# Optimization experiments

Hardware: AMD Instinct MI355X
Metric: run time of the kernel (lower is better)

## Reference

```python
import jax, jax.numpy as jnp
import numpy as np

B, T, C, A, D, H, W = 2, 16, 64, 64, 32, 32, 32  # batch, timepoints, channels, att_features, spatial


def setup_inputs() -> dict:
    key = jax.random.key(0)
    ks = jax.random.split(key, 7)
    s = 1.0 / np.sqrt(C)
    return {
        "x": jax.random.normal(ks[0], (B, T, C, D, H, W), dtype=jnp.float32),
        "Wk": jax.random.normal(ks[1], (A, C), dtype=jnp.float32) * s,
        "bk": jax.random.normal(ks[2], (A,), dtype=jnp.float32) * s,
        "Wq": jax.random.normal(ks[3], (A, C), dtype=jnp.float32) * s,
        "bq": jax.random.normal(ks[4], (A,), dtype=jnp.float32) * s,
        "Wv": jax.random.normal(ks[5], (C, C), dtype=jnp.float32) * s,
        "bv": jax.random.normal(ks[6], (C,), dtype=jnp.float32) * s,
    }


def reference(x, Wk, bk, Wq, bq, Wv, bv):
    # kernel=1 Conv3d == pointwise channel mixing. Project and move spatial
    # dims to the front exactly like movedim((3,4,5),(1,2,3)):
    # result layout [B, D, H, W, T, out_ch].
    def proj(Wt, bt):
        return jnp.einsum('btcdhw,oc->bdhwto', x, Wt) + bt

    k = proj(Wk, bk)  # [B,D,H,W,T,A]
    q = proj(Wq, bq)  # [B,D,H,W,T,A]
    v = proj(Wv, bv)  # [B,D,H,W,T,C]

    scale = 1.0 / np.sqrt(float(Wk.shape[0]))  # sqrt(att_features)
    att = jnp.einsum('bdhwta,bdhwsa->bdhwts', k, q) * scale  # [B,D,H,W,T,T]
    # norm = partial(softmax, dim=1) on the 6-D tensor -> softmax over spatial D axis
    att_map = jax.nn.softmax(att, axis=1)

    # features = (value^T @ att_map)^T: feat[...,s,c] = sum_t v[...,t,c] * att_map[...,t,s]
    feat = jnp.einsum('bdhwtc,bdhwts->bdhwsc', v, att_map)  # [B,D,H,W,T,C]
    # movedim((1,2,3),(3,4,5)): back to [B, T, C, D, H, W]
    return jnp.transpose(feat, (0, 4, 5, 1, 2, 3))
```

## Files before the change

### kernel.cpp

```cpp
#include <hip/hip_runtime.h>

typedef short v8s __attribute__((ext_vector_type(8)));
typedef float v4f __attribute__((ext_vector_type(4)));
typedef float v2f __attribute__((ext_vector_type(2)));

#define NSP 32768
#define XSTR 2056
#define WS_ZP_B 65536ull

__device__ __forceinline__ unsigned short f2bf(float f) {
  union { float f; unsigned u; } v; v.f = f;
  unsigned r = v.u + 0x7fffu + ((v.u >> 16) & 1u);
  return (unsigned short)(r >> 16);
}
__device__ __forceinline__ unsigned pk(float a, float b) {
  return (unsigned)f2bf(a) | ((unsigned)f2bf(b) << 16);
}

union UF8 { v8s v; unsigned u[4]; uint4 q; };


__global__ __launch_bounds__(512) void prep_kernel(
    const float* __restrict__ Wk, const float* __restrict__ bk,
    const float* __restrict__ Wq, const float* __restrict__ bq,
    const float* __restrict__ Wv, unsigned* __restrict__ ws) {
  __shared__ float sWk[4096], sWq[4096], sWv[4096], sbk[64], sbq[64];
  for (int i = threadIdx.x; i < 4096; i += 512) { sWk[i] = Wk[i]; sWq[i] = Wq[i]; sWv[i] = Wv[i]; }
  if (threadIdx.x < 64) { sbk[threadIdx.x] = bk[threadIdx.x]; sbq[threadIdx.x] = bq[threadIdx.x]; }
  __syncthreads();
  for (int task = threadIdx.x; task < 18 * 64; task += 512) {
    int f = task >> 6, lane = task & 63;
    int i16 = lane & 15, g = lane >> 4;
    unsigned short e[8];
    #pragma unroll
    for (int j = 0; j < 8; ++j) {
      int k = (((j >> 2) << 4) + 4 * g + (j & 3));
      float acc = 0.f;
      if (f < 8) {
        int row = ((f >> 1) << 4) + i16;
        int cc  = ((f & 1) << 5) + k;
        for (int a = 0; a < 64; ++a) acc += sWk[a * 64 + row] * sWq[a * 64 + cc];
      } else if (f < 10) {
        int c = ((f - 8) << 5) + k;
        if (i16 == 0)      { for (int a = 0; a < 64; ++a) acc += sWk[a * 64 + c] * sbq[a]; }
        else if (i16 == 1) { for (int a = 0; a < 64; ++a) acc += sbk[a] * sWq[a * 64 + c]; }
      } else {
        int c  = (((f - 10) >> 1) << 4) + i16;
        int cp = (((f - 10) & 1) << 5) + k;
        acc = sWv[c * 64 + cp];
      }
      e[j] = f2bf(acc);
    }
    unsigned* dst = ws + (size_t)(f * 64 + lane) * 4;
    dst[0] = e[0] | ((unsigned)e[1] << 16);
    dst[1] = e[2] | ((unsigned)e[3] << 16);
    dst[2] = e[4] | ((unsigned)e[5] << 16);
    dst[3] = e[6] | ((unsigned)e[7] << 16);
  }
  if (threadIdx.x == 0) {
    float beta = 0.f;
    for (int a = 0; a < 64; ++a) beta += sbk[a] * sbq[a];
    ((float*)ws)[18 * 256] = beta;
  }
}

#define S2L 0.18033688011112042f

#define DECODE256() \
  int bid = (int)blockIdx.x; \
  int b = bid & 1, dc = (bid >> 1) & 3, h = bid >> 3; \
  const int d0 = dc << 3; \
  const size_t base0 = (size_t)b * 33554432 + h * 32;

#define DECODE512() \
  int bid = (int)blockIdx.x; \
  int b = bid & 1, dcc = (bid >> 1) & 7, h = bid >> 4; \
  const int d0 = dcc << 2; \
  const size_t base0 = (size_t)b * 33554432 + h * 32;

#define STAGE_DEFS(BUF) \
  const int w2 = tid & 15; \
  const int rp0 = tid >> 4; \
  v2f sA[16], sB[16]; \
  auto issueH = [&](int d, int half) { \
    const float* xp = x + base0 + (size_t)d * 1024; \
    _Pragma("unroll") \
    for (int i = 0; i < 8; ++i) { \
      int rp = half * 256 + (i << 5) + rp0; \
      const float* r0 = xp + (size_t)(2 * rp) * NSP + 2 * w2; \
      sA[half * 8 + i] = *(const v2f*)r0; \
      sB[half * 8 + i] = *(const v2f*)(r0 + NSP); \
    } \
  }; \
  auto writeH = [&](int half) { \
    _Pragma("unroll") \
    for (int i = 0; i < 8; ++i) { \
      int rp = half * 256 + (i << 5) + rp0; \
      int t = rp >> 5, c = (rp & 31) << 1; \
      int off = (t << 7) + (((c << 1)) ^ ((t & 7) << 4)); \
      *(unsigned*)(&BUF[(2 * w2) * XSTR + off])     = pk(sA[half * 8 + i].x, sB[half * 8 + i].x); \
      *(unsigned*)(&BUF[(2 * w2 + 1) * XSTR + off]) = pk(sA[half * 8 + i].y, sB[half * 8 + i].y); \
    } \
  };

#define LOADX_DEF(BUF) \
  auto loadX = [&](int loc, v8s fX[2]) { \
    const unsigned char* bp = &BUF[loc * XSTR + (i16 << 7)]; \
    const int sw = (i16 & 7) << 4; \
    _Pragma("unroll") \
    for (int kc = 0; kc < 2; ++kc) { \
      union { v8s v; unsigned long long dd[2]; } u; \
      int o = (kc << 6) + (g << 3); \
      u.dd[0] = *(const unsigned long long*)(bp + (o ^ sw)); \
      u.dd[1] = *(const unsigned long long*)(bp + ((o + 32) ^ sw)); \
      fX[kc] = u.v; \
    } \
  };

#define LDF_DEF() \
  auto ldf = [&](int f) -> v8s { \
    union { v8s v; uint4 q; } u; \
    u.q = *(const uint4*)&Wm[(f << 8) + (lane << 2)]; \
    return u.v; \
  };

#define ATTOF_DEF() \
  auto attOf = [&](const v8s fX[2]) -> v4f { \
    v4f accW[4]; \
    _Pragma("unroll") \
    for (int tr = 0; tr < 4; ++tr) { \
      v8s m0 = ldf(2 * tr), m1 = ldf(2 * tr + 1); \
      v4f a = {0.f, 0.f, 0.f, 0.f}; \
      a = __builtin_amdgcn_mfma_f32_16x16x32_bf16(m0, fX[0], a, 0, 0, 0); \
      a = __builtin_amdgcn_mfma_f32_16x16x32_bf16(m1, fX[1], a, 0, 0, 0); \
      accW[tr] = a; \
    } \
    v8s u0 = ldf(8), u1 = ldf(9); \
    v4f au = {0.f, 0.f, 0.f, 0.f}; \
    au = __builtin_amdgcn_mfma_f32_16x16x32_bf16(u0, fX[0], au, 0, 0, 0); \
    au = __builtin_amdgcn_mfma_f32_16x16x32_bf16(u1, fX[1], au, 0, 0, 0); \
    float a1v = au[0] + beta; \
    float a2v = au[1]; \
    float a2s = __shfl(a2v, i16); \
    v4f att; \
    _Pragma("unroll") \
    for (int j = 0; j < 4; ++j) att[j] = __shfl(a1v, 4 * g + j) + a2s; \
    _Pragma("unroll") \
    for (int kc = 0; kc < 2; ++kc) { \
      UF8 w; \
      w.u[0] = pk(accW[2 * kc][0], accW[2 * kc][1]); \
      w.u[1] = pk(accW[2 * kc][2], accW[2 * kc][3]); \
      w.u[2] = pk(accW[2 * kc + 1][0], accW[2 * kc + 1][1]); \
      w.u[3] = pk(accW[2 * kc + 1][2], accW[2 * kc + 1][3]); \
      att = __builtin_amdgcn_mfma_f32_16x16x32_bf16(fX[kc], w.v, att, 0, 0, 0); \
    } \
    return att; \
  };

#define FEATQ(tn, FB) do { \
  _Pragma("unroll") \
  for (int l = 0; l < 4; ++l) { \
    int wq = 4 * wv + l; \
    UF8 fP; fP.u[0] = Pp[l][0]; fP.u[1] = Pp[l][1]; fP.u[2] = 0; fP.u[3] = 0; \
    UF8 fV; fV.u[0] = vp[l][2 * (tn)]; fV.u[1] = vp[l][2 * (tn) + 1]; fV.u[2] = 0; fV.u[3] = 0; \
    v4f ft = {0.f, 0.f, 0.f, 0.f}; \
    ft = __builtin_amdgcn_mfma_f32_16x16x32_bf16(fP.v, fV.v, ft, 0, 0, 0); \
    _Pragma("unroll") \
    for (int j = 0; j < 4; ++j) { \
      int r = (4 * g + j) * 16 + i16; \
      (FB)[r * 33 + (wq ^ g)] = ft[j]; \
    } \
  } \
} while (0)

__global__ __launch_bounds__(512) void pass1_z(
    const float* __restrict__ x, const unsigned* __restrict__ ws,
    float* __restrict__ zp) {
  __shared__ __align__(16) unsigned char Xbuf[32 * XSTR];
  __shared__ unsigned Wm[2560];

  const int tid = (int)threadIdx.x;
  const int lane = tid & 63, wv = tid >> 6;
  const int i16 = lane & 15, g = lane >> 4;
  DECODE256();

  for (int o = tid; o < 2560; o += 512) Wm[o] = ws[o];
  const float beta = ((const float*)ws)[4608];

  STAGE_DEFS(Xbuf);
  LOADX_DEF(Xbuf);
  LDF_DEF();
  ATTOF_DEF();

  float Z[4][4] = {};
  issueH(d0, 0); issueH(d0, 1);
  for (int ii = 0; ii < 8; ++ii) {
    const int d = d0 + ii;
    __syncthreads();
    writeH(0); writeH(1);
    __syncthreads();
    if (ii < 7) issueH(d + 1, 0);
    #pragma unroll
    for (int l = 0; l < 2; ++l) {
      v8s fX[2]; loadX(4 * wv + l, fX);
      v4f att = attOf(fX);
      #pragma unroll
      for (int j = 0; j < 4; ++j) Z[l][j] += exp2f(att[j] * S2L);
    }
    if (ii < 7) issueH(d + 1, 1);
    #pragma unroll
    for (int l = 2; l < 4; ++l) {
      v8s fX[2]; loadX(4 * wv + l, fX);
      v4f att = attOf(fX);
      #pragma unroll
      for (int j = 0; j < 4; ++j) Z[l][j] += exp2f(att[j] * S2L);
    }
  }
  const int locg = b * 1024 + h * 32 + 4 * wv;
  #pragma unroll
  for (int l = 0; l < 4; ++l)
    #pragma unroll
    for (int j = 0; j < 4; ++j)
      zp[(((size_t)dc * 2048 + locg + l) << 8) + (4 * g + j) * 16 + i16] = Z[l][j];
}

__global__ __launch_bounds__(512) void pass2_out(
    const float* __restrict__ x, const float* __restrict__ bv,
    const unsigned* __restrict__ ws, const float* __restrict__ zp,
    float* __restrict__ out) {
  __shared__ __align__(16) unsigned char UNI[67584];
  __shared__ unsigned Wm[2560];

  const int tid = (int)threadIdx.x;
  const int lane = tid & 63, wv = tid >> 6;
  const int i16 = lane & 15, g = lane >> 4;
  DECODE512();

  for (int o = tid; o < 2560; o += 512) Wm[o] = ws[o];
  const float beta = ((const float*)ws)[4608];
  float bvv[4];
  #pragma unroll
  for (int tn = 0; tn < 4; ++tn) bvv[tn] = bv[i16 + 16 * tn];

  float iZ[4][4];
  #pragma unroll
  for (int l = 0; l < 4; ++l) {
    const int locg = b * 1024 + h * 32 + 4 * wv + l;
    #pragma unroll
    for (int j = 0; j < 4; ++j) {
      float s = 0.f;
      #pragma unroll
      for (int c2 = 0; c2 < 4; ++c2)
        s += zp[(((size_t)c2 * 2048 + locg) << 8) + (4 * g + j) * 16 + i16];
      iZ[l][j] = 1.f / s;
    }
  }

  STAGE_DEFS(UNI);
  LOADX_DEF(UNI);
  LDF_DEF();
  ATTOF_DEF();

  float* FbA = (float*)UNI;
  float* FbB = FbA + 8448;
  const uint4* W4 = (const uint4*)ws;

  auto storeQ = [&](int tn, int d, const float* FB) {
    float* op = out + base0 + (size_t)d * 1024 + (size_t)(16 * tn) * NSP;
    const int w4 = tid & 7, rr = tid >> 3;
    #pragma unroll
    for (int it = 0; it < 4; ++it) {
      int r = (it << 6) + rr;
      const float* fp = &FB[r * 33 + (w4 << 2)];
      float4 val;
      val.x = fp[0 ^ it]; val.y = fp[1 ^ it]; val.z = fp[2 ^ it]; val.w = fp[3 ^ it];
      *(float4*)(op + (size_t)((r >> 4) * 64 + (r & 15)) * NSP + (w4 << 2)) = val;
    }
  };

  issueH(d0, 0); issueH(d0, 1);
  for (int ii = 0; ii < 4; ++ii) {
    const int d = d0 + ii;
    __syncthreads();
    writeH(0); writeH(1);
    __syncthreads();

    unsigned Pp[4][2], vp[4][8];
    #pragma unroll
    for (int l = 0; l < 4; ++l) {
      v8s fX[2]; loadX(4 * wv + l, fX);
      v4f att = attOf(fX);
      float p0 = exp2f(att[0] * S2L) * iZ[l][0];
      float p1 = exp2f(att[1] * S2L) * iZ[l][1];
      float p2 = exp2f(att[2] * S2L) * iZ[l][2];
      float p3 = exp2f(att[3] * S2L) * iZ[l][3];
      Pp[l][0] = pk(p0, p1); Pp[l][1] = pk(p2, p3);
      #pragma unroll
      for (int tn = 0; tn < 4; ++tn) {
        UF8 wa, wb;
        wa.q = W4[(10 + 2 * tn) * 64 + lane];
        wb.q = W4[(11 + 2 * tn) * 64 + lane];
        v4f a = {bvv[tn], bvv[tn], bvv[tn], bvv[tn]};
        a = __builtin_amdgcn_mfma_f32_16x16x32_bf16(fX[0], wa.v, a, 0, 0, 0);
        a = __builtin_amdgcn_mfma_f32_16x16x32_bf16(fX[1], wb.v, a, 0, 0, 0);
        vp[l][2 * tn] = pk(a[0], a[1]); vp[l][2 * tn + 1] = pk(a[2], a[3]);
      }
    }
    __syncthreads();

    FEATQ(0, FbA);
    __syncthreads();
    storeQ(0, d, FbA);
    if (ii < 3) issueH(d + 1, 0);
    FEATQ(1, FbB);
    __syncthreads();
    storeQ(1, d, FbB); FEATQ(2, FbA);
    __syncthreads();
    storeQ(2, d, FbA);
    if (ii < 3) issueH(d + 1, 1);
    FEATQ(3, FbB);
    __syncthreads();
    storeQ(3, d, FbB);
  }
}

extern "C" void kernel_launch(void* const* d_in, const int* in_sizes, int n_in,
                              void* d_out, int out_size, void* d_ws, size_t ws_size,
                              hipStream_t stream) {
  const float* x  = (const float*)d_in[0];
  const float* Wk = (const float*)d_in[1];
  const float* bk = (const float*)d_in[2];
  const float* Wq = (const float*)d_in[3];
  const float* bq = (const float*)d_in[4];
  const float* Wv = (const float*)d_in[5];
  const float* bv = (const float*)d_in[6];
  float* out = (float*)d_out;
  unsigned* ws = (unsigned*)d_ws;
  float* zp = (float*)((char*)d_ws + WS_ZP_B);

  prep_kernel<<<1, 512, 0, stream>>>(Wk, bk, Wq, bq, Wv, ws);
  pass1_z<<<256, 512, 0, stream>>>(x, ws, zp);
  pass2_out<<<512, 512, 0, stream>>>(x, bv, ws, zp, out);
}
```

Before: 304.9 us.

## Double-buffer staged x tiles in LDS and cache value weights in shared memory

Both passes now keep two LDS x buffers. The next depth slice is written into the spare buffer while the current one is consumed, which removes one barrier per iteration and lets the bf16 packing overlap with compute. Pass2 also copies the value-projection weights into LDS instead of reading them from global memory inside the MFMA loop. The cost is doubled LDS use, about 130+ KB per block, which limits blocks per CU to one. The staging register arrays shrink by half.

```diff
diff --git a/kernel.cpp b/kernel.cpp
--- a/kernel.cpp
+++ b/kernel.cpp
@@ -78,33 +78,33 @@
   const int d0 = dcc << 2; \
   const size_t base0 = (size_t)b * 33554432 + h * 32;
 
-#define STAGE_DEFS(BUF) \
+#define STAGE_DEFS() \
   const int w2 = tid & 15; \
   const int rp0 = tid >> 4; \
-  v2f sA[16], sB[16]; \
+  v2f sA[8], sB[8]; \
   auto issueH = [&](int d, int half) { \
     const float* xp = x + base0 + (size_t)d * 1024; \
     _Pragma("unroll") \
     for (int i = 0; i < 8; ++i) { \
       int rp = half * 256 + (i << 5) + rp0; \
       const float* r0 = xp + (size_t)(2 * rp) * NSP + 2 * w2; \
-      sA[half * 8 + i] = *(const v2f*)r0; \
-      sB[half * 8 + i] = *(const v2f*)(r0 + NSP); \
+      sA[i] = *(const v2f*)r0; \
+      sB[i] = *(const v2f*)(r0 + NSP); \
     } \
   }; \
-  auto writeH = [&](int half) { \
+  auto writeH = [&](unsigned char* BUF, int half) { \
     _Pragma("unroll") \
     for (int i = 0; i < 8; ++i) { \
       int rp = half * 256 + (i << 5) + rp0; \
       int t = rp >> 5, c = (rp & 31) << 1; \
       int off = (t << 7) + (((c << 1)) ^ ((t & 7) << 4)); \
-      *(unsigned*)(&BUF[(2 * w2) * XSTR + off])     = pk(sA[half * 8 + i].x, sB[half * 8 + i].x); \
-      *(unsigned*)(&BUF[(2 * w2 + 1) * XSTR + off]) = pk(sA[half * 8 + i].y, sB[half * 8 + i].y); \
-    } \
-  };
-
-#define LOADX_DEF(BUF) \
-  auto loadX = [&](int loc, v8s fX[2]) { \
+      *(unsigned*)(&BUF[(2 * w2) * XSTR + off])     = pk(sA[i].x, sB[i].x); \
+      *(unsigned*)(&BUF[(2 * w2 + 1) * XSTR + off]) = pk(sA[i].y, sB[i].y); \
+    } \
+  };
+
+#define LOADX_DEF() \
+  auto loadX = [&](const unsigned char* BUF, int loc, v8s fX[2]) { \
     const unsigned char* bp = &BUF[loc * XSTR + (i16 << 7)]; \
     const int sw = (i16 & 7) << 4; \
     _Pragma("unroll") \
@@ -176,7 +176,7 @@
 __global__ __launch_bounds__(512) void pass1_z(
     const float* __restrict__ x, const unsigned* __restrict__ ws,
     float* __restrict__ zp) {
-  __shared__ __align__(16) unsigned char Xbuf[32 * XSTR];
+  __shared__ __align__(16) unsigned char Xd[2][65792];
   __shared__ unsigned Wm[2560];
 
   const int tid = (int)threadIdx.x;
@@ -187,34 +187,37 @@
   for (int o = tid; o < 2560; o += 512) Wm[o] = ws[o];
   const float beta = ((const float*)ws)[4608];
 
-  STAGE_DEFS(Xbuf);
-  LOADX_DEF(Xbuf);
+  STAGE_DEFS();
+  LOADX_DEF();
   LDF_DEF();
   ATTOF_DEF();
 
   float Z[4][4] = {};
-  issueH(d0, 0); issueH(d0, 1);
+  issueH(d0, 0); writeH(Xd[0], 0);
+  issueH(d0, 1); writeH(Xd[0], 1);
+  __syncthreads();
   for (int ii = 0; ii < 8; ++ii) {
     const int d = d0 + ii;
-    __syncthreads();
-    writeH(0); writeH(1);
-    __syncthreads();
+    unsigned char* cur = Xd[ii & 1];
+    unsigned char* nxt = Xd[(ii & 1) ^ 1];
     if (ii < 7) issueH(d + 1, 0);
     #pragma unroll
     for (int l = 0; l < 2; ++l) {
-      v8s fX[2]; loadX(4 * wv + l, fX);
+      v8s fX[2]; loadX(cur, 4 * wv + l, fX);
       v4f att = attOf(fX);
       #pragma unroll
       for (int j = 0; j < 4; ++j) Z[l][j] += exp2f(att[j] * S2L);
     }
-    if (ii < 7) issueH(d + 1, 1);
+    if (ii < 7) { writeH(nxt, 0); issueH(d + 1, 1); }
     #pragma unroll
     for (int l = 2; l < 4; ++l) {
-      v8s fX[2]; loadX(4 * wv + l, fX);
+      v8s fX[2]; loadX(cur, 4 * wv + l, fX);
       v4f att = attOf(fX);
       #pragma unroll
       for (int j = 0; j < 4; ++j) Z[l][j] += exp2f(att[j] * S2L);
     }
+    if (ii < 7) writeH(nxt, 1);
+    __syncthreads();
   }
   const int locg = b * 1024 + h * 32 + 4 * wv;
   #pragma unroll
@@ -228,15 +231,15 @@
     const float* __restrict__ x, const float* __restrict__ bv,
     const unsigned* __restrict__ ws, const float* __restrict__ zp,
     float* __restrict__ out) {
-  __shared__ __align__(16) unsigned char UNI[67584];
-  __shared__ unsigned Wm[2560];
+  __shared__ __align__(16) unsigned char Xd[2][67584];
+  __shared__ unsigned Wm[4608];
 
   const int tid = (int)threadIdx.x;
   const int lane = tid & 63, wv = tid >> 6;
   const int i16 = lane & 15, g = lane >> 4;
   DECODE512();
 
-  for (int o = tid; o < 2560; o += 512) Wm[o] = ws[o];
+  for (int o = tid; o < 4608; o += 512) Wm[o] = ws[o];
   const float beta = ((const float*)ws)[4608];
   float bvv[4];
   #pragma unroll
@@ -256,14 +259,10 @@
     }
   }
 
-  STAGE_DEFS(UNI);
-  LOADX_DEF(UNI);
+  STAGE_DEFS();
+  LOADX_DEF();
   LDF_DEF();
   ATTOF_DEF();
-
-  float* FbA = (float*)UNI;
-  float* FbB = FbA + 8448;
-  const uint4* W4 = (const uint4*)ws;
 
   auto storeQ = [&](int tn, int d, const float* FB) {
     float* op = out + base0 + (size_t)d * 1024 + (size_t)(16 * tn) * NSP;
@@ -278,17 +277,20 @@
     }
   };
 
-  issueH(d0, 0); issueH(d0, 1);
+  issueH(d0, 0); writeH(Xd[0], 0);
+  issueH(d0, 1); writeH(Xd[0], 1);
   for (int ii = 0; ii < 4; ++ii) {
     const int d = d0 + ii;
-    __syncthreads();
-    writeH(0); writeH(1);
+    unsigned char* A = Xd[ii & 1];
+    unsigned char* B = Xd[(ii & 1) ^ 1];
     __syncthreads();
 
     unsigned Pp[4][2], vp[4][8];
+    if (ii < 3) issueH(d + 1, 0);
     #pragma unroll
     for (int l = 0; l < 4; ++l) {
-      v8s fX[2]; loadX(4 * wv + l, fX);
+      if (l == 2 && ii < 3) { writeH(B, 0); issueH(d + 1, 1); }
+      v8s fX[2]; loadX(A, 4 * wv + l, fX);
       v4f att = attOf(fX);
       float p0 = exp2f(att[0] * S2L) * iZ[l][0];
       float p1 = exp2f(att[1] * S2L) * iZ[l][1];
@@ -297,28 +299,25 @@
       Pp[l][0] = pk(p0, p1); Pp[l][1] = pk(p2, p3);
       #pragma unroll
       for (int tn = 0; tn < 4; ++tn) {
-        UF8 wa, wb;
-        wa.q = W4[(10 + 2 * tn) * 64 + lane];
-        wb.q = W4[(11 + 2 * tn) * 64 + lane];
+        v8s wa = ldf(10 + 2 * tn), wb = ldf(11 + 2 * tn);
         v4f a = {bvv[tn], bvv[tn], bvv[tn], bvv[tn]};
-        a = __builtin_amdgcn_mfma_f32_16x16x32_bf16(fX[0], wa.v, a, 0, 0, 0);
-        a = __builtin_amdgcn_mfma_f32_16x16x32_bf16(fX[1], wb.v, a, 0, 0, 0);
+        a = __builtin_amdgcn_mfma_f32_16x16x32_bf16(fX[0], wa, a, 0, 0, 0);
+        a = __builtin_amdgcn_mfma_f32_16x16x32_bf16(fX[1], wb, a, 0, 0, 0);
         vp[l][2 * tn] = pk(a[0], a[1]); vp[l][2 * tn + 1] = pk(a[2], a[3]);
       }
     }
-    __syncthreads();
-
+    if (ii < 3) writeH(B, 1);
+    __syncthreads();
+
+    float* FbA = (float*)A;
+    float* FbB = FbA + 8448;
     FEATQ(0, FbA);
     __syncthreads();
-    storeQ(0, d, FbA);
-    if (ii < 3) issueH(d + 1, 0);
-    FEATQ(1, FbB);
+    storeQ(0, d, FbA); FEATQ(1, FbB);
     __syncthreads();
     storeQ(1, d, FbB); FEATQ(2, FbA);
     __syncthreads();
-    storeQ(2, d, FbA);
-    if (ii < 3) issueH(d + 1, 1);
-    FEATQ(3, FbB);
+    storeQ(2, d, FbA); FEATQ(3, FbB);
     __syncthreads();
     storeQ(3, d, FbB);
   }
@@ -330,8 +329,8 @@
   const float* x  = (const float*)d_in[0];
   const float* Wk = (const float*)d_in[1];
   const float* bk = (const float*)d_in[2];
+  const float* bq = (const float*)d_in[4];
   const float* Wq = (const float*)d_in[3];
-  const float* bq = (const float*)d_in[4];
   const float* Wv = (const float*)d_in[5];
   const float* bv = (const float*)d_in[6];
   float* out = (float*)d_out;
```

Result: faster. 267.7 us (-12.2%).
